# Performance work log

Measured on AMD Instinct MI355X. Metric: run time of the kernel, lower is better.

## Reference

```python
import jax, jax.numpy as jnp
import numpy as np

K = 4        # maximum_fertility + 1
OOV_ID = 1
HIDDEN = 512


def setup_inputs() -> dict:
    key = jax.random.key(0)
    ks = jax.random.split(key, 8)
    B, S, D, E, H, V = 4, 128, 512, 256, HIDDEN, 32000
    return {
        "embedded_input": jax.random.normal(ks[0], (B, S, D), jnp.float32),
        "input_mask": jnp.ones((B, S), jnp.int32),
        "emb_table": jax.random.normal(ks[1], (V, E), jnp.float32) * 0.02,
        "W_ih": jax.random.normal(ks[2], (4 * H, D + E), jnp.float32) * 0.02,
        "b_ih": jax.random.normal(ks[3], (4 * H,), jnp.float32) * 0.02,
        "W_hh": jax.random.normal(ks[4], (4 * H, H), jnp.float32) * 0.02,
        "b_hh": jax.random.normal(ks[5], (4 * H,), jnp.float32) * 0.02,
        "W_out": jax.random.normal(ks[6], (V, H), jnp.float32) * 0.02,
        "b_out": jax.random.normal(ks[7], (V,), jnp.float32) * 0.02,
    }


def reference(embedded_input, input_mask, emb_table, W_ih, b_ih, W_hh, b_hh, W_out, b_out):
    B, S, D = embedded_input.shape
    V, E = emb_table.shape
    H = HIDDEN
    N = B * S
    x = embedded_input.reshape(N, D)                      # (N, D)
    h0 = jnp.zeros((N, H), embedded_input.dtype)
    c0 = jnp.zeros((N, H), embedded_input.dtype)
    # initial last_output: one-hot at OOV id (prob mass 1.0 on oov)
    last0 = jnp.zeros((N, V), embedded_input.dtype).at[:, OOV_ID].set(1.0)

    def step(carry, _):
        h, c, last = carry
        # embedding_bag soft mix over full vocab == weighted sum == matmul
        emb_last = last @ emb_table                        # (N, E)
        inp = jnp.concatenate([x, emb_last], axis=1)       # (N, D+E)
        gates = inp @ W_ih.T + b_ih + h @ W_hh.T + b_hh    # (N, 4H)
        i, f, g, o = jnp.split(gates, 4, axis=1)           # torch LSTMCell gate order
        i = jax.nn.sigmoid(i)
        f = jax.nn.sigmoid(f)
        g = jnp.tanh(g)
        o = jax.nn.sigmoid(o)
        c_new = f * c + i * g
        h_new = o * jnp.tanh(c_new)
        # dropout=0 / eval -> dropout mask is all ones (no-op)
        logits = h_new @ W_out.T + b_out                   # (N, V)
        logp = jax.nn.log_softmax(logits, axis=-1)
        return (h_new, c_new, jnp.exp(logp)), logp

    _, outs = jax.lax.scan(step, (h0, c0, last0), None, length=K)  # (K, N, V)
    return outs.transpose(1, 0, 2).reshape(B, S, K, V)
```

## Files before the change

### kernel.cpp

```cpp
#include <hip/hip_runtime.h>
#include <hip/hip_bf16.h>
#include <math.h>

#define N_ROWS 512
#define D_IN   512
#define E_EMB  256
#define H_DIM  512
#define G_DIM  2048
#define V_DIM  32000
#define IN_LD  1280
#define K_STEPS 4
#define OOV_ID 1
#define TBK 64
#define EMB_SPLIT 25
#define EMB_CHUNK 1280
#define SEGSTRIDE 512

typedef __attribute__((ext_vector_type(4))) float f32x4;
typedef __attribute__((ext_vector_type(8))) short bf16x8;

__device__ inline short f2b(float v) {
    __hip_bfloat16 h = __float2bfloat16(v);
    return *reinterpret_cast<short*>(&h);
}

__device__ inline void gload_lds(const short* g, short* l) {
    __builtin_amdgcn_global_load_lds(
        (const __attribute__((address_space(1))) void*)g,
        (__attribute__((address_space(3))) void*)l, 16, 0, 0);
}

template<int TBM, int TBN, int WR_, int WC_, int MODE, int STATS>
__global__ __launch_bounds__(WR_ * WC_ * 64) void k_gemm(
    const short* __restrict__ A, int lda,
    const short* __restrict__ B, int ldb,
    const float* __restrict__ bias,
    float* __restrict__ C, size_t ldc, int Kc,
    float2* __restrict__ stats,
    float* __restrict__ cstate, short* __restrict__ hdst)
{
    constexpr int NW = WR_ * WC_;
    constexpr int WMT = TBM / WR_, WNT = TBN / WC_;
    constexpr int WM = WMT / 16, WN = WNT / 16;
    __shared__ short As[TBM * 64];
    __shared__ short Bs[TBN * 64];
    const int tid = threadIdx.x;
    const int lane = tid & 63, wid = tid >> 6;
    const int wr = wid % WR_, wc = wid / WR_;
    const int quad = lane >> 4, l16 = lane & 15;
    const int m0 = blockIdx.y * TBM, n0 = blockIdx.x * TBN;
    const int kbase = blockIdx.z * Kc;
    const int lrow = lane >> 3;
    const int lsw  = ((lane & 7) ^ lrow) * 8;

    f32x4 acc[WM][WN];
#pragma unroll
    for (int i = 0; i < WM; ++i)
#pragma unroll
        for (int j = 0; j < WN; ++j)
#pragma unroll
            for (int r = 0; r < 4; ++r) acc[i][j][r] = 0.0f;

    for (int kt = 0; kt < Kc; kt += TBK) {
        const int k0 = kbase + kt;
#pragma unroll
        for (int ch = wid; ch < TBM / 8; ch += NW)
            gload_lds(&A[(size_t)(m0 + ch * 8 + lrow) * lda + k0 + lsw], &As[ch * 512]);
#pragma unroll
        for (int ch = wid; ch < TBN / 8; ch += NW)
            gload_lds(&B[(size_t)(n0 + ch * 8 + lrow) * ldb + k0 + lsw], &Bs[ch * 512]);
        __syncthreads();
#pragma unroll
        for (int ks = 0; ks < 2; ++ks) {
            bf16x8 af[WM], bfv[WN];
#pragma unroll
            for (int i = 0; i < WM; ++i) {
                int rr = wr * WMT + i * 16 + l16;
                af[i] = *(const bf16x8*)&As[rr * 64 + (((ks * 4 + quad) ^ (l16 & 7)) * 8)];
            }
#pragma unroll
            for (int j = 0; j < WN; ++j) {
                int rr = wc * WNT + j * 16 + l16;
                bfv[j] = *(const bf16x8*)&Bs[rr * 64 + (((ks * 4 + quad) ^ (l16 & 7)) * 8)];
            }
#pragma unroll
            for (int i = 0; i < WM; ++i)
#pragma unroll
                for (int j = 0; j < WN; ++j)
                    acc[i][j] = __builtin_amdgcn_mfma_f32_16x16x32_bf16(af[i], bfv[j], acc[i][j], 0, 0, 0);
        }
        __syncthreads();
    }

    if constexpr (MODE == 1) {
#pragma unroll
        for (int i = 0; i < WM; ++i)
#pragma unroll
            for (int j = 0; j < WN; ++j) {
                const int n = n0 + wc * WNT + j * 16 + l16;
#pragma unroll
                for (int r = 0; r < 4; ++r) {
                    const int m = m0 + wr * WMT + i * 16 + quad * 4 + r;
                    atomicAdd(&C[(size_t)m * ldc + n], acc[i][j][r]);
                }
            }
    } else if constexpr (MODE == 2) {
        float bv[WN];
#pragma unroll
        for (int j = 0; j < WN; ++j) bv[j] = bias[n0 + j * 16 + l16];
        const int jj = (n0 >> 2) + l16;
#pragma unroll
        for (int i = 0; i < WM; ++i) {
#pragma unroll
            for (int r = 0; r < 4; ++r) {
                const int m = m0 + wr * WMT + i * 16 + quad * 4 + r;
                float gi = acc[i][0][r] + bv[0];
                float gf = acc[i][1][r] + bv[1];
                float gg = acc[i][2][r] + bv[2];
                float go = acc[i][3][r] + bv[3];
                float i_ = 1.0f / (1.0f + expf(-gi));
                float f_ = 1.0f / (1.0f + expf(-gf));
                float g_ = tanhf(gg);
                float o_ = 1.0f / (1.0f + expf(-go));
                const size_t ci = (size_t)m * H_DIM + jj;
                float cn = f_ * cstate[ci] + i_ * g_;
                cstate[ci] = cn;
                hdst[(size_t)m * IN_LD + (D_IN + E_EMB) + jj] = f2b(o_ * tanhf(cn));
            }
        }
    } else {
        float bv[WN];
#pragma unroll
        for (int j = 0; j < WN; ++j) bv[j] = bias[n0 + wc * WNT + j * 16 + l16];
#pragma unroll
        for (int i = 0; i < WM; ++i) {
            if constexpr (!STATS) {
#pragma unroll
                for (int j = 0; j < WN; ++j) {
                    const int n = n0 + wc * WNT + j * 16 + l16;
#pragma unroll
                    for (int r = 0; r < 4; ++r) {
                        const int m = m0 + wr * WMT + i * 16 + quad * 4 + r;
                        C[(size_t)m * ldc + n] = acc[i][j][r] + bv[j];
                    }
                }
            } else {
                float rm[4] = {-1e30f, -1e30f, -1e30f, -1e30f};
                float rs[4] = {0.f, 0.f, 0.f, 0.f};
#pragma unroll
                for (int j = 0; j < WN; ++j)
#pragma unroll
                    for (int r = 0; r < 4; ++r)
                        rm[r] = fmaxf(rm[r], acc[i][j][r] + bv[j]);
#pragma unroll
                for (int j = 0; j < WN; ++j) {
                    const int n = n0 + wc * WNT + j * 16 + l16;
#pragma unroll
                    for (int r = 0; r < 4; ++r) {
                        const int m = m0 + wr * WMT + i * 16 + quad * 4 + r;
                        float z = acc[i][j][r] + bv[j];
                        rs[r] += __expf(z - rm[r]);
                        C[(size_t)m * ldc + n] = z;
                    }
                }
#pragma unroll
                for (int mask = 1; mask < 16; mask <<= 1) {
#pragma unroll
                    for (int r = 0; r < 4; ++r) {
                        float om = __shfl_xor(rm[r], mask);
                        float os = __shfl_xor(rs[r], mask);
                        float nm = fmaxf(rm[r], om);
                        rs[r] = rs[r] * __expf(rm[r] - nm) + os * __expf(om - nm);
                        rm[r] = nm;
                    }
                }
                if (l16 == 0) {
                    const int seg = (n0 + wc * WNT) >> 6;
#pragma unroll
                    for (int r = 0; r < 4; ++r) {
                        const int m = m0 + wr * WMT + i * 16 + quad * 4 + r;
                        stats[(size_t)m * SEGSTRIDE + seg] = make_float2(rm[r], rs[r]);
                    }
                }
            }
        }
    }
}

__global__ __launch_bounds__(256) void k_prep(
    const float* __restrict__ x, const float* __restrict__ emb_table,
    const float* __restrict__ W_ih, const float* __restrict__ W_hh,
    const float* __restrict__ b_ih, const float* __restrict__ b_hh,
    const float* __restrict__ W_out,
    short* __restrict__ Abuf, short* __restrict__ Wg, float* __restrict__ bsum,
    short* __restrict__ Wout16, float* __restrict__ c)
{
    const int idx0 = blockIdx.x * 256 + threadIdx.x;
    const int gs = gridDim.x * 256;
    const float4* W4 = (const float4*)W_out;
    for (int i = idx0; i < V_DIM * H_DIM / 4; i += gs) {
        float4 v = W4[i];
        short4 o;
        o.x = f2b(v.x); o.y = f2b(v.y); o.z = f2b(v.z); o.w = f2b(v.w);
        ((short4*)Wout16)[i] = o;
    }
    for (int i = idx0; i < G_DIM * IN_LD; i += gs) {
        int rp = i / IN_LD, k = i - rp * IN_LD;
        int j = ((rp >> 6) << 4) | (rp & 15);
        int gate = (rp >> 4) & 3;
        int g = gate * H_DIM + j;
        float v = (k < D_IN + E_EMB) ? W_ih[(size_t)g * (D_IN + E_EMB) + k]
                                     : W_hh[(size_t)g * H_DIM + (k - (D_IN + E_EMB))];
        Wg[i] = f2b(v);
    }
    for (int i = idx0; i < G_DIM; i += gs) {
        int j = ((i >> 6) << 4) | (i & 15);
        int gate = (i >> 4) & 3;
        int g = gate * H_DIM + j;
        bsum[i] = b_ih[g] + b_hh[g];
    }
    for (int i = idx0; i < N_ROWS * IN_LD; i += gs) {
        int n = i / IN_LD, col = i - n * IN_LD;
        float v;
        if (col < D_IN)              v = x[(size_t)n * D_IN + col];
        else if (col < D_IN + E_EMB) v = emb_table[(size_t)OOV_ID * E_EMB + (col - D_IN)];
        else                         v = 0.0f;
        Abuf[i] = f2b(v);
    }
    for (int i = idx0; i < N_ROWS * H_DIM; i += gs) c[i] = 0.0f;
}

__global__ __launch_bounds__(256) void k_trans(const float* __restrict__ emb,
                                               short* __restrict__ embT)
{
    __shared__ float tile[64][65];
    const int v0 = blockIdx.x * 64, e0 = blockIdx.y * 64;
    const int tid = threadIdx.x;
#pragma unroll
    for (int i = 0; i < 16; ++i) {
        int idx = tid + i * 256;
        int vr = idx >> 6, ec = idx & 63;
        tile[vr][ec] = emb[(size_t)(v0 + vr) * E_EMB + e0 + ec];
    }
    __syncthreads();
#pragma unroll
    for (int i = 0; i < 16; ++i) {
        int idx = tid + i * 256;
        int er = idx >> 6, vc = idx & 63;
        embT[(size_t)(e0 + er) * V_DIM + v0 + vc] = f2b(tile[vc][er]);
    }
}

__global__ __launch_bounds__(256) void k_cvt_emb(const float* __restrict__ emb_acc,
                                                 short* __restrict__ Abuf)
{
    int idx = blockIdx.x * 256 + threadIdx.x;
    int n = idx >> 8, e = idx & 255;
    Abuf[(size_t)n * IN_LD + D_IN + e] = f2b(emb_acc[idx]);
}

__global__ __launch_bounds__(256) void k_lse(const float2* __restrict__ stats,
                                             float* __restrict__ lse,
                                             float* __restrict__ emb_acc,
                                             int feed)
{
    const int tid = threadIdx.x;
    const int lane = tid & 63, wid = tid >> 6;
    const int n = blockIdx.x * 4 + wid;

    float m = -1e30f, s = 0.0f;
    for (int sg = lane; sg < V_DIM / 64; sg += 64) {
        float2 p = stats[(size_t)n * SEGSTRIDE + sg];
        float nm = fmaxf(m, p.x);
        s = s * __expf(m - nm) + p.y * __expf(p.x - nm);
        m = nm;
    }
#pragma unroll
    for (int mask = 32; mask > 0; mask >>= 1) {
        float om = __shfl_xor(m, mask);
        float os = __shfl_xor(s, mask);
        float nm = fmaxf(m, om);
        s = s * __expf(m - nm) + os * __expf(om - nm);
        m = nm;
    }
    if (lane == 0) lse[n] = m + __logf(s);

    if (feed) {
        ((float4*)&emb_acc[(size_t)n * E_EMB])[lane] = make_float4(0.f, 0.f, 0.f, 0.f);
    }
}

__global__ __launch_bounds__(256) void k_finish(float* __restrict__ out,
                                                short* __restrict__ last,
                                                const float* __restrict__ lse,
                                                int step, int feed)
{
    const int n = blockIdx.y;
    const float l = lse[n];
    float4* row4 = (float4*)(out + ((size_t)n * K_STEPS + step) * V_DIM);
    short4* prow = (short4*)(last + (size_t)n * V_DIM);
    const int c0 = blockIdx.x * 1024 + threadIdx.x;
#pragma unroll
    for (int i = 0; i < 4; ++i) {
        const int c = c0 + i * 256;
        if (c < V_DIM / 4) {
            float4 xv = row4[c];
            xv.x -= l; xv.y -= l; xv.z -= l; xv.w -= l;
            row4[c] = xv;
            if (feed) {
                short4 p;
                p.x = f2b(__expf(xv.x)); p.y = f2b(__expf(xv.y));
                p.z = f2b(__expf(xv.z)); p.w = f2b(__expf(xv.w));
                prow[c] = p;
            }
        }
    }
}

extern "C" void kernel_launch(void* const* d_in, const int* in_sizes, int n_in,
                              void* d_out, int out_size, void* d_ws, size_t ws_size,
                              hipStream_t stream) {
    (void)in_sizes; (void)n_in; (void)out_size; (void)ws_size;
    const float* x       = (const float*)d_in[0];
    const float* emb_tab = (const float*)d_in[2];
    const float* W_ih    = (const float*)d_in[3];
    const float* b_ih    = (const float*)d_in[4];
    const float* W_hh    = (const float*)d_in[5];
    const float* b_hh    = (const float*)d_in[6];
    const float* W_out   = (const float*)d_in[7];
    const float* b_out   = (const float*)d_in[8];
    float* out = (float*)d_out;

    char* ws = (char*)d_ws;
    short* Abuf   = (short*)ws;  ws += (size_t)N_ROWS * IN_LD * sizeof(short);
    float* c      = (float*)ws;  ws += (size_t)N_ROWS * H_DIM * sizeof(float);
    short* last   = (short*)ws;  ws += (size_t)N_ROWS * V_DIM * sizeof(short);
    short* Wout16 = (short*)ws;  ws += (size_t)V_DIM * H_DIM * sizeof(short);
    short* Wg     = (short*)ws;  ws += (size_t)G_DIM * IN_LD * sizeof(short);
    float* bsum   = (float*)ws;  ws += (size_t)G_DIM * sizeof(float);
    short* embT   = (short*)ws;  ws += (size_t)E_EMB * V_DIM * sizeof(short);
    float* emb_acc= (float*)ws;  ws += (size_t)N_ROWS * E_EMB * sizeof(float);
    float2* stats = (float2*)ws; ws += (size_t)N_ROWS * SEGSTRIDE * sizeof(float2);
    float* lse    = (float*)ws;  ws += (size_t)N_ROWS * sizeof(float);

    k_prep<<<2048, 256, 0, stream>>>(x, emb_tab, W_ih, W_hh, b_ih, b_hh, W_out,
                                     Abuf, Wg, bsum, Wout16, c);
    k_trans<<<dim3(V_DIM / 64, E_EMB / 64), 256, 0, stream>>>(emb_tab, embT);

    for (int t = 0; t < K_STEPS; ++t) {
        if (t > 0) {
            k_gemm<128, 256, 2, 4, 1, 0><<<dim3(1, N_ROWS / 128, EMB_SPLIT), 512, 0, stream>>>(
                last, V_DIM, embT, V_DIM, nullptr, emb_acc, E_EMB, EMB_CHUNK,
                nullptr, nullptr, nullptr);
            k_cvt_emb<<<N_ROWS * E_EMB / 256, 256, 0, stream>>>(emb_acc, Abuf);
        }
        k_gemm<64, 64, 4, 1, 2, 0><<<dim3(G_DIM / 64, N_ROWS / 64, 1), 256, 0, stream>>>(
            Abuf, IN_LD, Wg, IN_LD, bsum, nullptr, 0, IN_LD, nullptr, c, Abuf);
        k_gemm<256, 128, 4, 2, 0, 1><<<dim3(V_DIM / 128, N_ROWS / 256, 1), 512, 0, stream>>>(
            Abuf + (D_IN + E_EMB), IN_LD, Wout16, H_DIM, b_out,
            out + (size_t)t * V_DIM, (size_t)K_STEPS * V_DIM, H_DIM, stats,
            nullptr, nullptr);
        const int feed = (t < K_STEPS - 1) ? 1 : 0;
        k_lse<<<N_ROWS / 4, 256, 0, stream>>>(stats, lse, emb_acc, feed);
        k_finish<<<dim3(8, N_ROWS), 256, 0, stream>>>(out, last, lse, t, feed);
    }
}
```

Measured before the change: 768.9 us.

## Stage logits in fp16 scratch and replace atomic split-K with partial-sum reduction

The output-projection GEMM now writes logits as fp16 into a scratch buffer instead of fp32 into the final output. The finish kernel reads them back, subtracts the log-sum-exp and writes fp32 log-probs once, which avoids a read-modify-write of the large fp32 output. The embedding split-K GEMM doubles its split count and writes per-split partial sums, which a separate kernel then reduces; this replaces the atomicAdd accumulation and the zeroing step. The trade-offs are fp16 rounding of the logits before normalisation and extra partial-sum traffic.

```diff
diff --git a/kernel.cpp b/kernel.cpp
--- a/kernel.cpp
+++ b/kernel.cpp
@@ -12,12 +12,13 @@
 #define K_STEPS 4
 #define OOV_ID 1
 #define TBK 64
-#define EMB_SPLIT 25
-#define EMB_CHUNK 1280
+#define EMB_SPLIT 50
+#define EMB_CHUNK 640
 #define SEGSTRIDE 512
 
 typedef __attribute__((ext_vector_type(4))) float f32x4;
 typedef __attribute__((ext_vector_type(8))) short bf16x8;
+typedef __attribute__((ext_vector_type(8))) _Float16 f16x8;
 
 __device__ inline short f2b(float v) {
     __hip_bfloat16 h = __float2bfloat16(v);
@@ -30,7 +31,7 @@
         (__attribute__((address_space(3))) void*)l, 16, 0, 0);
 }
 
-template<int TBM, int TBN, int WR_, int WC_, int MODE, int STATS>
+template<int TBM, int TBN, int WR_, int WC_, int MODE>
 __global__ __launch_bounds__(WR_ * WC_ * 64) void k_gemm(
     const short* __restrict__ A, int lda,
     const short* __restrict__ B, int ldb,
@@ -92,7 +93,8 @@
         __syncthreads();
     }
 
-    if constexpr (MODE == 1) {
+    if constexpr (MODE == 3) {
+        float* Cp = C + (size_t)blockIdx.z * N_ROWS * ldc;
 #pragma unroll
         for (int i = 0; i < WM; ++i)
 #pragma unroll
@@ -101,7 +103,7 @@
 #pragma unroll
                 for (int r = 0; r < 4; ++r) {
                     const int m = m0 + wr * WMT + i * 16 + quad * 4 + r;
-                    atomicAdd(&C[(size_t)m * ldc + n], acc[i][j][r]);
+                    Cp[(size_t)m * ldc + n] = acc[i][j][r];
                 }
             }
     } else if constexpr (MODE == 2) {
@@ -128,62 +130,66 @@
                 hdst[(size_t)m * IN_LD + (D_IN + E_EMB) + jj] = f2b(o_ * tanhf(cn));
             }
         }
+    } else if constexpr (MODE == 4) {
+        _Float16* Ch = (_Float16*)C;
+        float bv[WN];
+#pragma unroll
+        for (int j = 0; j < WN; ++j) bv[j] = bias[n0 + wc * WNT + j * 16 + l16];
+#pragma unroll
+        for (int i = 0; i < WM; ++i) {
+            float rm[4] = {-1e30f, -1e30f, -1e30f, -1e30f};
+            float rs[4] = {0.f, 0.f, 0.f, 0.f};
+#pragma unroll
+            for (int j = 0; j < WN; ++j)
+#pragma unroll
+                for (int r = 0; r < 4; ++r)
+                    rm[r] = fmaxf(rm[r], acc[i][j][r] + bv[j]);
+#pragma unroll
+            for (int j = 0; j < WN; ++j) {
+                const int n = n0 + wc * WNT + j * 16 + l16;
+#pragma unroll
+                for (int r = 0; r < 4; ++r) {
+                    const int m = m0 + wr * WMT + i * 16 + quad * 4 + r;
+                    float z = acc[i][j][r] + bv[j];
+                    rs[r] += __expf(z - rm[r]);
+                    Ch[(size_t)m * ldc + n] = (_Float16)z;
+                }
+            }
+#pragma unroll
+            for (int mask = 1; mask < 16; mask <<= 1) {
+#pragma unroll
+                for (int r = 0; r < 4; ++r) {
+                    float om = __shfl_xor(rm[r], mask);
+                    float os = __shfl_xor(rs[r], mask);
+                    float nm = fmaxf(rm[r], om);
+                    rs[r] = rs[r] * __expf(rm[r] - nm) + os * __expf(om - nm);
+                    rm[r] = nm;
+                }
+            }
+            if (l16 == 0) {
+                const int seg = (n0 + wc * WNT) >> 6;
+#pragma unroll
+                for (int r = 0; r < 4; ++r) {
+                    const int m = m0 + wr * WMT + i * 16 + quad * 4 + r;
+                    stats[(size_t)m * SEGSTRIDE + seg] = make_float2(rm[r], rs[r]);
+                }
+            }
+        }
     } else {
         float bv[WN];
 #pragma unroll
         for (int j = 0; j < WN; ++j) bv[j] = bias[n0 + wc * WNT + j * 16 + l16];
 #pragma unroll
-        for (int i = 0; i < WM; ++i) {
-            if constexpr (!STATS) {
-#pragma unroll
-                for (int j = 0; j < WN; ++j) {
-                    const int n = n0 + wc * WNT + j * 16 + l16;
-#pragma unroll
-                    for (int r = 0; r < 4; ++r) {
-                        const int m = m0 + wr * WMT + i * 16 + quad * 4 + r;
-                        C[(size_t)m * ldc + n] = acc[i][j][r] + bv[j];
-                    }
-                }
-            } else {
-                float rm[4] = {-1e30f, -1e30f, -1e30f, -1e30f};
-                float rs[4] = {0.f, 0.f, 0.f, 0.f};
-#pragma unroll
-                for (int j = 0; j < WN; ++j)
-#pragma unroll
-                    for (int r = 0; r < 4; ++r)
-                        rm[r] = fmaxf(rm[r], acc[i][j][r] + bv[j]);
-#pragma unroll
-                for (int j = 0; j < WN; ++j) {
-                    const int n = n0 + wc * WNT + j * 16 + l16;
-#pragma unroll
-                    for (int r = 0; r < 4; ++r) {
-                        const int m = m0 + wr * WMT + i * 16 + quad * 4 + r;
-                        float z = acc[i][j][r] + bv[j];
-                        rs[r] += __expf(z - rm[r]);
-                        C[(size_t)m * ldc + n] = z;
-                    }
-                }
-#pragma unroll
-                for (int mask = 1; mask < 16; mask <<= 1) {
-#pragma unroll
-                    for (int r = 0; r < 4; ++r) {
-                        float om = __shfl_xor(rm[r], mask);
-                        float os = __shfl_xor(rs[r], mask);
-                        float nm = fmaxf(rm[r], om);
-                        rs[r] = rs[r] * __expf(rm[r] - nm) + os * __expf(om - nm);
-                        rm[r] = nm;
-                    }
-                }
-                if (l16 == 0) {
-                    const int seg = (n0 + wc * WNT) >> 6;
-#pragma unroll
-                    for (int r = 0; r < 4; ++r) {
-                        const int m = m0 + wr * WMT + i * 16 + quad * 4 + r;
-                        stats[(size_t)m * SEGSTRIDE + seg] = make_float2(rm[r], rs[r]);
-                    }
-                }
-            }
-        }
+        for (int i = 0; i < WM; ++i)
+#pragma unroll
+            for (int j = 0; j < WN; ++j) {
+                const int n = n0 + wc * WNT + j * 16 + l16;
+#pragma unroll
+                for (int r = 0; r < 4; ++r) {
+                    const int m = m0 + wr * WMT + i * 16 + quad * 4 + r;
+                    C[(size_t)m * ldc + n] = acc[i][j][r] + bv[j];
+                }
+            }
     }
 }
 
@@ -251,18 +257,22 @@
     }
 }
 
-__global__ __launch_bounds__(256) void k_cvt_emb(const float* __restrict__ emb_acc,
-                                                 short* __restrict__ Abuf)
+__global__ __launch_bounds__(256) void k_embred(const float* __restrict__ ep,
+                                                short* __restrict__ Abuf)
 {
     int idx = blockIdx.x * 256 + threadIdx.x;
     int n = idx >> 8, e = idx & 255;
-    Abuf[(size_t)n * IN_LD + D_IN + e] = f2b(emb_acc[idx]);
+    float s0 = 0.f, s1 = 0.f;
+#pragma unroll
+    for (int z = 0; z < EMB_SPLIT; z += 2) {
+        s0 += ep[((size_t)z * N_ROWS + n) * E_EMB + e];
+        s1 += ep[((size_t)(z + 1) * N_ROWS + n) * E_EMB + e];
+    }
+    Abuf[(size_t)n * IN_LD + D_IN + e] = f2b(s0 + s1);
 }
 
 __global__ __launch_bounds__(256) void k_lse(const float2* __restrict__ stats,
-                                             float* __restrict__ lse,
-                                             float* __restrict__ emb_acc,
-                                             int feed)
+                                             float* __restrict__ lse)
 {
     const int tid = threadIdx.x;
     const int lane = tid & 63, wid = tid >> 6;
@@ -284,34 +294,35 @@
         m = nm;
     }
     if (lane == 0) lse[n] = m + __logf(s);
-
-    if (feed) {
-        ((float4*)&emb_acc[(size_t)n * E_EMB])[lane] = make_float4(0.f, 0.f, 0.f, 0.f);
-    }
-}
-
-__global__ __launch_bounds__(256) void k_finish(float* __restrict__ out,
+}
+
+__global__ __launch_bounds__(256) void k_finish(const _Float16* __restrict__ zbuf,
+                                                float* __restrict__ out,
                                                 short* __restrict__ last,
                                                 const float* __restrict__ lse,
                                                 int step, int feed)
 {
     const int n = blockIdx.y;
     const float l = lse[n];
+    const f16x8* zr = (const f16x8*)(zbuf + (size_t)n * V_DIM);
     float4* row4 = (float4*)(out + ((size_t)n * K_STEPS + step) * V_DIM);
-    short4* prow = (short4*)(last + (size_t)n * V_DIM);
-    const int c0 = blockIdx.x * 1024 + threadIdx.x;
-#pragma unroll
-    for (int i = 0; i < 4; ++i) {
-        const int c = c0 + i * 256;
-        if (c < V_DIM / 4) {
-            float4 xv = row4[c];
-            xv.x -= l; xv.y -= l; xv.z -= l; xv.w -= l;
-            row4[c] = xv;
+    bf16x8* prow = (bf16x8*)(last + (size_t)n * V_DIM);
+#pragma unroll
+    for (int it = 0; it < 2; ++it) {
+        const int slot = threadIdx.x + it * 256;
+        if (slot < 500) {
+            const int cidx = blockIdx.x * 500 + slot;
+            f16x8 zv = zr[cidx];
+            float lp[8];
+#pragma unroll
+            for (int k = 0; k < 8; ++k) lp[k] = (float)zv[k] - l;
+            row4[cidx * 2]     = make_float4(lp[0], lp[1], lp[2], lp[3]);
+            row4[cidx * 2 + 1] = make_float4(lp[4], lp[5], lp[6], lp[7]);
             if (feed) {
-                short4 p;
-                p.x = f2b(__expf(xv.x)); p.y = f2b(__expf(xv.y));
-                p.z = f2b(__expf(xv.z)); p.w = f2b(__expf(xv.w));
-                prow[c] = p;
+                bf16x8 p;
+#pragma unroll
+                for (int k = 0; k < 8; ++k) p[k] = f2b(__expf(lp[k]));
+                prow[cidx] = p;
             }
         }
     }
@@ -339,9 +350,12 @@
     short* Wg     = (short*)ws;  ws += (size_t)G_DIM * IN_LD * sizeof(short);
     float* bsum   = (float*)ws;  ws += (size_t)G_DIM * sizeof(float);
     short* embT   = (short*)ws;  ws += (size_t)E_EMB * V_DIM * sizeof(short);
-    float* emb_acc= (float*)ws;  ws += (size_t)N_ROWS * E_EMB * sizeof(float);
     float2* stats = (float2*)ws; ws += (size_t)N_ROWS * SEGSTRIDE * sizeof(float2);
     float* lse    = (float*)ws;  ws += (size_t)N_ROWS * sizeof(float);
+    ws = (char*)(((size_t)ws + 255) & ~(size_t)255);
+    _Float16* zbuf = (_Float16*)ws;
+    float* epart   = (float*)ws;
+    ws += (size_t)N_ROWS * V_DIM * sizeof(_Float16);
 
     k_prep<<<2048, 256, 0, stream>>>(x, emb_tab, W_ih, W_hh, b_ih, b_hh, W_out,
                                      Abuf, Wg, bsum, Wout16, c);
@@ -349,19 +363,18 @@
 
     for (int t = 0; t < K_STEPS; ++t) {
         if (t > 0) {
-            k_gemm<128, 256, 2, 4, 1, 0><<<dim3(1, N_ROWS / 128, EMB_SPLIT), 512, 0, stream>>>(
-                last, V_DIM, embT, V_DIM, nullptr, emb_acc, E_EMB, EMB_CHUNK,
+            k_gemm<128, 256, 2, 4, 3><<<dim3(1, N_ROWS / 128, EMB_SPLIT), 512, 0, stream>>>(
+                last, V_DIM, embT, V_DIM, nullptr, epart, E_EMB, EMB_CHUNK,
                 nullptr, nullptr, nullptr);
-            k_cvt_emb<<<N_ROWS * E_EMB / 256, 256, 0, stream>>>(emb_acc, Abuf);
-        }
-        k_gemm<64, 64, 4, 1, 2, 0><<<dim3(G_DIM / 64, N_ROWS / 64, 1), 256, 0, stream>>>(
+            k_embred<<<N_ROWS * E_EMB / 256, 256, 0, stream>>>(epart, Abuf);
+        }
+        k_gemm<64, 64, 4, 1, 2><<<dim3(G_DIM / 64, N_ROWS / 64, 1), 256, 0, stream>>>(
             Abuf, IN_LD, Wg, IN_LD, bsum, nullptr, 0, IN_LD, nullptr, c, Abuf);
-        k_gemm<256, 128, 4, 2, 0, 1><<<dim3(V_DIM / 128, N_ROWS / 256, 1), 512, 0, stream>>>(
+        k_gemm<256, 128, 4, 2, 4><<<dim3(V_DIM / 128, N_ROWS / 256, 1), 512, 0, stream>>>(
             Abuf + (D_IN + E_EMB), IN_LD, Wout16, H_DIM, b_out,
-            out + (size_t)t * V_DIM, (size_t)K_STEPS * V_DIM, H_DIM, stats,
-            nullptr, nullptr);
+            (float*)zbuf, V_DIM, H_DIM, stats, nullptr, nullptr);
         const int feed = (t < K_STEPS - 1) ? 1 : 0;
-        k_lse<<<N_ROWS / 4, 256, 0, stream>>>(stats, lse, emb_acc, feed);
-        k_finish<<<dim3(8, N_ROWS), 256, 0, stream>>>(out, last, lse, t, feed);
-    }
-}
+        k_lse<<<N_ROWS / 4, 256, 0, stream>>>(stats, lse);
+        k_finish<<<dim3(8, N_ROWS), 256, 0, stream>>>(zbuf, out, last, lse, t, feed);
+    }
+}
```

Measured after the change: 692.8 us. -9.9%, faster.
